# Kernel tuning notes

Measured on AMD Instinct MI355X. Metric: run time of the kernel, lower is better.

## Reference

```python
import jax, jax.numpy as jnp
import numpy as np
import math

B, N, E, D = 8, 2048, 2048, 128
MAX_K = 8
HYPER_DIM = 128
LN_EPS = 1e-5


def _sinusoidal_pe(max_pos, dim):
    pe = np.zeros((max_pos, dim), dtype=np.float32)
    position = np.arange(max_pos, dtype=np.float32)[:, None]
    div_term = np.exp(np.arange(0, dim, 2, dtype=np.float32) * (-math.log(10000.0) / dim))
    pe[:, 0::2] = np.sin(position * div_term)
    pe[:, 1::2] = np.cos(position * div_term)
    return jnp.asarray(pe)


def setup_inputs() -> dict:
    key = jax.random.key(0)
    ks = jax.random.split(key, 24)
    s = 0.05
    inp = {
        'x_v': jax.random.normal(ks[0], (B, N, D), jnp.float32),
        'x_e': jax.random.normal(ks[1], (B, E, D), jnp.float32),
        'incidence': (jax.random.uniform(ks[2], (B, N, E), jnp.float32) < 0.01).astype(jnp.float32),
        'suffix_normalizer': jax.random.uniform(ks[3], (B, N), jnp.float32) * 20.0,
        'edge_orders': 1 + jax.random.randint(ks[4], (B, E), 0, MAX_K),
        'node_mask': jax.random.randint(ks[5], (B, N), 0, 2) > 0,
        'edge_mask': jax.random.randint(ks[6], (B, E), 0, 2) > 0,
        'pe1_table': _sinusoidal_pe(MAX_K + 1, D),
        'pe2_table': _sinusoidal_pe(2, D),
        'bias_b': jax.random.uniform(ks[7], (1, D), jnp.float32, -1, 1) / math.sqrt(D),
    }
    i = 8
    for m in ('mlp1', 'mlp2', 'mlp3'):
        inp[m + '_W1'] = jax.random.normal(ks[i], (D, HYPER_DIM), jnp.float32) * s; i += 1
        inp[m + '_b1'] = jnp.zeros((HYPER_DIM,), jnp.float32)
        inp[m + '_W2'] = jax.random.normal(ks[i], (HYPER_DIM, D), jnp.float32) * s; i += 1
        inp[m + '_b2'] = jnp.zeros((D,), jnp.float32)
    for n in ('norm1', 'norm2', 'norm3'):
        inp[n + '_g'] = jnp.ones((D,), jnp.float32)
        inp[n + '_b'] = jnp.zeros((D,), jnp.float32)
    return inp


def _ln(x, g, b):
    mu = jnp.mean(x, axis=-1, keepdims=True)
    var = jnp.mean(jnp.square(x - mu), axis=-1, keepdims=True)
    return (x - mu) * jax.lax.rsqrt(var + LN_EPS) * g + b


def _mlp(x, W1, b1, W2, b2):
    return jax.nn.relu(x @ W1 + b1) @ W2 + b2


def reference(x_v, x_e, incidence, suffix_normalizer, edge_orders, node_mask, edge_mask,
              pe1_table, pe2_table, bias_b,
              mlp1_W1, mlp1_b1, mlp1_W2, mlp1_b2,
              mlp2_W1, mlp2_b1, mlp2_W2, mlp2_b2,
              mlp3_W1, mlp3_b1, mlp3_W2, mlp3_b2,
              norm1_g, norm1_b, norm2_g, norm2_b, norm3_g, norm3_b):
    nm = node_mask[..., None]  # [B,N,1]
    em = edge_mask[..., None]  # [B,E,1]
    x_v = jnp.where(nm, x_v, 0.0)
    x_e = jnp.where(em, x_e, 0.0)
    pe1_k1 = pe1_table[1][None, None, :]          # [1,1,D]
    pe1_k = pe1_table[edge_orders]                # [B,E,D]
    x_v = x_v + _mlp(_ln(x_v, norm1_g, norm1_b) + pe1_k1, mlp1_W1, mlp1_b1, mlp1_W2, mlp1_b2)
    x_e = x_e + _mlp(_ln(x_e, norm1_g, norm1_b) + pe1_k, mlp1_W1, mlp1_b1, mlp1_W2, mlp1_b2)
    x_v = jnp.where(nm, x_v, 0.0)
    x_e = jnp.where(em, x_e, 0.0)
    agg = jnp.einsum('bne,bed->bnd', incidence, x_e)
    x1 = x_v + agg / (1.0 + suffix_normalizer[..., None])
    pe2_s1 = pe2_table[1][None, None, :]
    x1 = x1 + _mlp(_ln(x1, norm2_g, norm2_b) + pe2_s1, mlp2_W1, mlp2_b1, mlp2_W2, mlp2_b2)
    x = jnp.where(nm, x1, 0.0)
    x = x + _mlp(_ln(x, norm3_g, norm3_b), mlp3_W1, mlp3_b1, mlp3_W2, mlp3_b2)
    x = x + bias_b
    x = jnp.where(nm, x, 0.0)
    return x
```

## Files before the change

kernel.cpp:

```cpp
#include <hip/hip_runtime.h>
#include <stdint.h>

#define BB 8
#define NN 2048
#define EE 2048
#define DD 128
#define ROWS 32
#define RBP 132
#define NTHREADS 256
#define WMAT_U32 8192

typedef __attribute__((ext_vector_type(8))) short bf16x8;
typedef __attribute__((ext_vector_type(4))) float f32x4;

__device__ inline unsigned bf16rne(float f) {
    unsigned u = __float_as_uint(f);
    return (u + 0x7fffu + ((u >> 16) & 1u)) >> 16;
}
__device__ inline float bf16lo(unsigned u) { return __uint_as_float(u << 16); }
__device__ inline float bf16hi(unsigned u) { return __uint_as_float(u & 0xffff0000u); }

#define SWZ(b) ((b) ^ ((((b) >> 8) & 7) << 4))

struct __align__(16) Smem {
    float rowbuf[ROWS][RBP];
    unsigned h[ROWS * DD / 2];
    unsigned scw[4][64];
    int rmask[ROWS];
    int ords[ROWS];
};

__global__ __launch_bounds__(NTHREADS) void convert_w_kernel(
    const float* __restrict__ W11, const float* __restrict__ W12,
    const float* __restrict__ W21, const float* __restrict__ W22,
    const float* __restrict__ W31, const float* __restrict__ W32,
    unsigned* __restrict__ WT) {
    int tid = blockIdx.x * NTHREADS + threadIdx.x;
    if (tid >= 6 * WMAT_U32) return;
    int mat = tid >> 13;
    int idx = tid & (WMAT_U32 - 1);
    int n = idx >> 6, j = idx & 63;
    const float* W = mat == 0 ? W11 : mat == 1 ? W12 : mat == 2 ? W21
                   : mat == 3 ? W22 : mat == 4 ? W31 : W32;
    float a = W[(2 * j) * DD + n];
    float b = W[(2 * j + 1) * DD + n];
    WT[tid] = bf16rne(a) | (bf16rne(b) << 16);
}

__device__ inline void block_load_rows(Smem& s, const float* __restrict__ src,
                                       const int* __restrict__ mask) {
    int t = threadIdx.x;
    for (int idx = t; idx < ROWS * 32; idx += NTHREADS) {
        int r = idx >> 5, c4 = (idx & 31) * 4;
        float4 v = make_float4(0.f, 0.f, 0.f, 0.f);
        if (mask[r] != 0) v = *(const float4*)&src[r * DD + c4];
        *(float4*)&s.rowbuf[r][c4] = v;
    }
    __syncthreads();
}

__device__ inline void block_ln(Smem& s, const float* __restrict__ gw,
                                const float* __restrict__ bw,
                                const float* __restrict__ pe_base, bool per_row_pe) {
    int t = threadIdx.x;
    int gr = t >> 3, g = t & 7;
    int base = g * 16;
    float x[16];
    float4* xp = (float4*)x;
    xp[0] = *(const float4*)&s.rowbuf[gr][base + 0];
    xp[1] = *(const float4*)&s.rowbuf[gr][base + 4];
    xp[2] = *(const float4*)&s.rowbuf[gr][base + 8];
    xp[3] = *(const float4*)&s.rowbuf[gr][base + 12];
    float s1 = 0.f, s2 = 0.f;
    #pragma unroll
    for (int i = 0; i < 16; i++) { s1 += x[i]; s2 += x[i] * x[i]; }
    #pragma unroll
    for (int off = 1; off < 8; off <<= 1) {
        s1 += __shfl_xor(s1, off, 64);
        s2 += __shfl_xor(s2, off, 64);
    }
    float mu = s1 * (1.f / 128.f);
    float var = s2 * (1.f / 128.f) - mu * mu;
    float rstd = rsqrtf(var + 1e-5f);
    const float* pe = nullptr;
    if (pe_base) pe = per_row_pe ? (pe_base + (size_t)s.ords[gr] * DD) : pe_base;
    unsigned p[8];
    #pragma unroll
    for (int j = 0; j < 8; j++) {
        int k0 = base + 2 * j;
        float v0 = (x[2 * j] - mu) * rstd * gw[k0] + bw[k0];
        float v1 = (x[2 * j + 1] - mu) * rstd * gw[k0 + 1] + bw[k0 + 1];
        if (pe) { v0 += pe[k0]; v1 += pe[k0 + 1]; }
        p[j] = bf16rne(v0) | (bf16rne(v1) << 16);
    }
    char* hb = (char*)s.h;
    int byte0 = gr * 256 + g * 32;
    uint4 lo = make_uint4(p[0], p[1], p[2], p[3]);
    uint4 hi = make_uint4(p[4], p[5], p[6], p[7]);
    *(uint4*)(hb + SWZ(byte0)) = lo;
    *(uint4*)(hb + SWZ(byte0 + 16)) = hi;
    __syncthreads();
}

template <bool TO_H>
__device__ inline void block_mm(Smem& s, const unsigned* __restrict__ WT,
                                const float* __restrict__ bias) {
    int t = threadIdx.x;
    int w = t >> 6, l = t & 63;
    int lm = l & 15, lk = l >> 4;
    bf16x8 bfr[2][4];
    const uint4* wt4 = (const uint4*)WT;
    #pragma unroll
    for (int nbl = 0; nbl < 2; nbl++) {
        int n = w * 32 + nbl * 16 + lm;
        #pragma unroll
        for (int kb = 0; kb < 4; kb++) {
            uint4 u = wt4[n * 16 + kb * 4 + lk];
            bfr[nbl][kb] = *(bf16x8*)&u;
        }
    }
    const char* hb = (const char*)s.h;
    bf16x8 afr[2][4];
    #pragma unroll
    for (int mb = 0; mb < 2; mb++) {
        int row = mb * 16 + lm;
        #pragma unroll
        for (int kb = 0; kb < 4; kb++) {
            afr[mb][kb] = *(const bf16x8*)(hb + SWZ(row * 256 + kb * 64 + lk * 16));
        }
    }
    f32x4 acc[2][2];
    #pragma unroll
    for (int mb = 0; mb < 2; mb++)
        #pragma unroll
        for (int nbl = 0; nbl < 2; nbl++)
            acc[mb][nbl] = (f32x4){0.f, 0.f, 0.f, 0.f};
    #pragma unroll
    for (int kb = 0; kb < 4; kb++)
        #pragma unroll
        for (int mb = 0; mb < 2; mb++)
            #pragma unroll
            for (int nbl = 0; nbl < 2; nbl++)
                acc[mb][nbl] = __builtin_amdgcn_mfma_f32_16x16x32_bf16(
                    afr[mb][kb], bfr[nbl][kb], acc[mb][nbl], 0, 0, 0);
    float bcol0 = bias[w * 32 + lm];
    float bcol1 = bias[w * 32 + 16 + lm];
    __syncthreads();
    if (TO_H) {
        char* hw = (char*)s.h;
        #pragma unroll
        for (int mb = 0; mb < 2; mb++)
            #pragma unroll
            for (int nbl = 0; nbl < 2; nbl++) {
                int col = w * 32 + nbl * 16 + lm;
                float bc = nbl ? bcol1 : bcol0;
                #pragma unroll
                for (int j = 0; j < 4; j++) {
                    int row = mb * 16 + lk * 4 + j;
                    float v = fmaxf(acc[mb][nbl][j] + bc, 0.f);
                    *(unsigned short*)(hw + SWZ(row * 256 + col * 2)) =
                        (unsigned short)bf16rne(v);
                }
            }
    } else {
        #pragma unroll
        for (int mb = 0; mb < 2; mb++)
            #pragma unroll
            for (int nbl = 0; nbl < 2; nbl++) {
                int col = w * 32 + nbl * 16 + lm;
                float bc = nbl ? bcol1 : bcol0;
                #pragma unroll
                for (int j = 0; j < 4; j++) {
                    int row = mb * 16 + lk * 4 + j;
                    s.rowbuf[row][col] += acc[mb][nbl][j] + bc;
                }
            }
    }
    __syncthreads();
}

__device__ inline void block_gather(Smem& s, int rowbase, int bb,
                                    const float* __restrict__ inc,
                                    const unsigned* __restrict__ e2pk,
                                    const float* __restrict__ sn) {
    int t = threadIdx.x;
    int w = t >> 6, l = t & 63;
    unsigned long long lmlt = (1ull << l) - 1ull;
    unsigned* sc = s.scw[w];
    const unsigned* e2b = e2pk + (size_t)bb * (EE * (DD / 2));
    for (int r = w; r < ROWS; r += 4) {
        if (s.rmask[r] == 0) continue;
        int grow = rowbase + r;
        const float4* ir = (const float4*)(inc + (size_t)grow * EE);
        float4 v[8];
        #pragma unroll
        for (int i = 0; i < 8; i++) v[i] = ir[l + 64 * i];
        int total = 0;
        #pragma unroll
        for (int i = 0; i < 8; i++) {
            #pragma unroll
            for (int c = 0; c < 4; c++) {
                float val = (c == 0) ? v[i].x : (c == 1) ? v[i].y : (c == 2) ? v[i].z : v[i].w;
                bool nz = (val != 0.f);
                unsigned long long msk = __ballot(nz);
                if (nz) {
                    int pos = total + __popcll(msk & lmlt);
                    if (pos < 64) sc[pos] = (unsigned)((l + 64 * i) * 4 + c);
                }
                total += __popcll(msk);
            }
        }
        if (total > 64) total = 64;
        asm volatile("s_waitcnt lgkmcnt(0)" ::: "memory");
        unsigned pk = (l < total) ? sc[l] : 0u;
        float ax = 0.f, ay = 0.f;
        for (int j0 = 0; j0 < total; j0 += 8) {
            int nn = total - j0;
            unsigned uv[8];
            #pragma unroll
            for (int u = 0; u < 8; u++) {
                unsigned e = __shfl(pk, j0 + u, 64);
                uv[u] = (u < nn) ? e2b[(size_t)e * 64 + l] : 0u;
            }
            #pragma unroll
            for (int u = 0; u < 8; u++) { ax += bf16lo(uv[u]); ay += bf16hi(uv[u]); }
        }
        float inv = 1.f / (1.f + sn[grow]);
        float2* rb = (float2*)&s.rowbuf[r][2 * l];
        float2 cur = *rb;
        cur.x += ax * inv;
        cur.y += ay * inv;
        *rb = cur;
    }
    __syncthreads();
}

__global__ __launch_bounds__(NTHREADS) void edge_kernel(
    const float* __restrict__ x_e, const int* __restrict__ emask,
    const int* __restrict__ eord, const float* __restrict__ pe1,
    const float* __restrict__ n1g, const float* __restrict__ n1b,
    const unsigned* __restrict__ WT,
    const float* __restrict__ b11, const float* __restrict__ b12,
    unsigned* __restrict__ e2pk) {
    __shared__ Smem s;
    int bid = blockIdx.x;
    int bb = bid & 7;
    int e0 = (bid >> 3) * ROWS;
    int rowbase = bb * EE + e0;
    int t = threadIdx.x;
    if (t < ROWS) {
        s.rmask[t] = emask[rowbase + t];
        int o = eord[rowbase + t];
        s.ords[t] = o < 0 ? 0 : (o > 8 ? 8 : o);
    }
    block_load_rows(s, x_e + (size_t)rowbase * DD, emask + rowbase);
    block_ln(s, n1g, n1b, pe1, true);
    block_mm<true>(s, WT + 0 * WMAT_U32, b11);
    block_mm<false>(s, WT + 1 * WMAT_U32, b12);
    unsigned* dst = e2pk + (size_t)rowbase * (DD / 2);
    for (int idx = t; idx < ROWS * 16; idx += NTHREADS) {
        int r = idx >> 4, q = idx & 15;
        uint4 o = make_uint4(0u, 0u, 0u, 0u);
        if (s.rmask[r] != 0) {
            const float* rp = &s.rowbuf[r][q * 8];
            o.x = bf16rne(rp[0]) | (bf16rne(rp[1]) << 16);
            o.y = bf16rne(rp[2]) | (bf16rne(rp[3]) << 16);
            o.z = bf16rne(rp[4]) | (bf16rne(rp[5]) << 16);
            o.w = bf16rne(rp[6]) | (bf16rne(rp[7]) << 16);
        }
        *(uint4*)&dst[r * 64 + q * 4] = o;
    }
}

__global__ __launch_bounds__(NTHREADS) void node_kernel(
    const float* __restrict__ x_v, const int* __restrict__ nmask,
    const float* __restrict__ inc, const float* __restrict__ sn,
    const float* __restrict__ pe1, const float* __restrict__ pe2,
    const float* __restrict__ biasb,
    const float* __restrict__ n1g, const float* __restrict__ n1b,
    const float* __restrict__ n2g, const float* __restrict__ n2b,
    const float* __restrict__ n3g, const float* __restrict__ n3b,
    const unsigned* __restrict__ WT,
    const float* __restrict__ b11, const float* __restrict__ b12,
    const float* __restrict__ b21, const float* __restrict__ b22,
    const float* __restrict__ b31, const float* __restrict__ b32,
    const unsigned* __restrict__ e2pk, float* __restrict__ out) {
    __shared__ Smem s;
    int bid = blockIdx.x;
    int bb = bid & 7;
    int n0 = (bid >> 3) * ROWS;
    int rowbase = bb * NN + n0;
    int t = threadIdx.x;
    if (t < ROWS) s.rmask[t] = nmask[rowbase + t];
    block_load_rows(s, x_v + (size_t)rowbase * DD, nmask + rowbase);
    block_ln(s, n1g, n1b, pe1 + DD, false);
    block_mm<true>(s, WT + 0 * WMAT_U32, b11);
    block_mm<false>(s, WT + 1 * WMAT_U32, b12);
    block_gather(s, rowbase, bb, inc, e2pk, sn);
    block_ln(s, n2g, n2b, pe2 + DD, false);
    block_mm<true>(s, WT + 2 * WMAT_U32, b21);
    block_mm<false>(s, WT + 3 * WMAT_U32, b22);
    block_ln(s, n3g, n3b, nullptr, false);
    block_mm<true>(s, WT + 4 * WMAT_U32, b31);
    block_mm<false>(s, WT + 5 * WMAT_U32, b32);
    for (int idx = t; idx < ROWS * 32; idx += NTHREADS) {
        int r = idx >> 5, c4 = (idx & 31) * 4;
        float4 v = make_float4(0.f, 0.f, 0.f, 0.f);
        if (s.rmask[r] != 0) {
            v = *(const float4*)&s.rowbuf[r][c4];
            float4 bbv = *(const float4*)&biasb[c4];
            v.x += bbv.x; v.y += bbv.y; v.z += bbv.z; v.w += bbv.w;
        }
        *(float4*)&out[(size_t)(rowbase + r) * DD + c4] = v;
    }
}

extern "C" void kernel_launch(void* const* d_in, const int* in_sizes, int n_in,
                              void* d_out, int out_size, void* d_ws, size_t ws_size,
                              hipStream_t stream) {
    const float* x_v   = (const float*)d_in[0];
    const float* x_e   = (const float*)d_in[1];
    const float* inc   = (const float*)d_in[2];
    const float* sn    = (const float*)d_in[3];
    const int*   eord  = (const int*)d_in[4];
    const int*   nmask = (const int*)d_in[5];
    const int*   emask = (const int*)d_in[6];
    const float* pe1   = (const float*)d_in[7];
    const float* pe2   = (const float*)d_in[8];
    const float* biasb = (const float*)d_in[9];
    const float* W11   = (const float*)d_in[10];
    const float* b11   = (const float*)d_in[11];
    const float* W12   = (const float*)d_in[12];
    const float* b12   = (const float*)d_in[13];
    const float* W21   = (const float*)d_in[14];
    const float* b21   = (const float*)d_in[15];
    const float* W22   = (const float*)d_in[16];
    const float* b22   = (const float*)d_in[17];
    const float* W31   = (const float*)d_in[18];
    const float* b31   = (const float*)d_in[19];
    const float* W32   = (const float*)d_in[20];
    const float* b32   = (const float*)d_in[21];
    const float* n1g   = (const float*)d_in[22];
    const float* n1b   = (const float*)d_in[23];
    const float* n2g   = (const float*)d_in[24];
    const float* n2b   = (const float*)d_in[25];
    const float* n3g   = (const float*)d_in[26];
    const float* n3b   = (const float*)d_in[27];

    unsigned* e2pk = (unsigned*)d_ws;
    unsigned* WT   = e2pk + (size_t)BB * EE * (DD / 2);
    float*    out  = (float*)d_out;

    dim3 blk(NTHREADS);
    convert_w_kernel<<<dim3((6 * WMAT_U32 + NTHREADS - 1) / NTHREADS), blk, 0, stream>>>(
        W11, W12, W21, W22, W31, W32, WT);
    edge_kernel<<<dim3(BB * EE / ROWS), blk, 0, stream>>>(
        x_e, emask, eord, pe1, n1g, n1b, WT, b11, b12, e2pk);
    node_kernel<<<dim3(BB * NN / ROWS), blk, 0, stream>>>(
        x_v, nmask, inc, sn, pe1, pe2, biasb,
        n1g, n1b, n2g, n2b, n3g, n3b,
        WT, b11, b12, b21, b22, b31, b32,
        e2pk, out);
}
```

Measured before the change: 68.61 us.

## Move incidence scan into edge kernel as extra blocks producing compact neighbor lists

The dense incidence scan that builds per-node nonzero edge lists moves out of the node kernel. It now runs in extra blocks appended to the edge kernel launch, so the 128 MiB incidence read can overlap with the edge MLP work. Lists and counts go to workspace, and the node kernel only reads the compact lists before gathering. This costs extra global writes and reads for the lists, and the edge-kernel blocks now compete with the scan blocks for bandwidth.

```diff
diff --git a/kernel.cpp b/kernel.cpp
--- a/kernel.cpp
+++ b/kernel.cpp
@@ -9,6 +9,8 @@
 #define RBP 132
 #define NTHREADS 256
 #define WMAT_U32 8192
+#define SCANB 2048
+#define LCAP 64
 
 typedef __attribute__((ext_vector_type(8))) short bf16x8;
 typedef __attribute__((ext_vector_type(4))) float f32x4;
@@ -179,18 +181,16 @@
     __syncthreads();
 }
 
-__device__ inline void block_gather(Smem& s, int rowbase, int bb,
-                                    const float* __restrict__ inc,
-                                    const unsigned* __restrict__ e2pk,
-                                    const float* __restrict__ sn) {
-    int t = threadIdx.x;
-    int w = t >> 6, l = t & 63;
+__device__ inline void scan_rows(Smem& s, const float* __restrict__ inc,
+                                 const int* __restrict__ nmask,
+                                 unsigned* __restrict__ lists, int* __restrict__ cnts,
+                                 int wid, int nwaves) {
+    int l = threadIdx.x & 63;
+    int w = threadIdx.x >> 6;
+    unsigned* sc = s.scw[w];
     unsigned long long lmlt = (1ull << l) - 1ull;
-    unsigned* sc = s.scw[w];
-    const unsigned* e2b = e2pk + (size_t)bb * (EE * (DD / 2));
-    for (int r = w; r < ROWS; r += 4) {
-        if (s.rmask[r] == 0) continue;
-        int grow = rowbase + r;
+    for (int grow = wid; grow < BB * NN; grow += nwaves) {
+        if (nmask[grow] == 0) continue;
         const float4* ir = (const float4*)(inc + (size_t)grow * EE);
         float4 v[8];
         #pragma unroll
@@ -205,17 +205,37 @@
                 unsigned long long msk = __ballot(nz);
                 if (nz) {
                     int pos = total + __popcll(msk & lmlt);
-                    if (pos < 64) sc[pos] = (unsigned)((l + 64 * i) * 4 + c);
+                    if (pos < LCAP) sc[pos] = (unsigned)((l + 64 * i) * 4 + c);
                 }
                 total += __popcll(msk);
             }
         }
-        if (total > 64) total = 64;
+        if (total > LCAP) total = LCAP;
         asm volatile("s_waitcnt lgkmcnt(0)" ::: "memory");
-        unsigned pk = (l < total) ? sc[l] : 0u;
+        if (l < 16) {
+            uint4 q = *(const uint4*)&sc[4 * l];
+            *(uint4*)&lists[(size_t)grow * LCAP + 4 * l] = q;
+        }
+        if (l == 0) cnts[grow] = total;
+    }
+}
+
+__device__ inline void block_gather(Smem& s, int rowbase, int bb,
+                                    const unsigned* __restrict__ lists,
+                                    const int* __restrict__ cnts,
+                                    const unsigned* __restrict__ e2pk,
+                                    const float* __restrict__ sn) {
+    int t = threadIdx.x;
+    int w = t >> 6, l = t & 63;
+    const unsigned* e2b = e2pk + (size_t)bb * (EE * (DD / 2));
+    for (int r = w; r < ROWS; r += 4) {
+        if (s.rmask[r] == 0) continue;
+        int grow = rowbase + r;
+        int cnt = cnts[grow];
+        unsigned pk = (l < cnt) ? lists[(size_t)grow * LCAP + l] : 0u;
         float ax = 0.f, ay = 0.f;
-        for (int j0 = 0; j0 < total; j0 += 8) {
-            int nn = total - j0;
+        for (int j0 = 0; j0 < cnt; j0 += 8) {
+            int nn = cnt - j0;
             unsigned uv[8];
             #pragma unroll
             for (int u = 0; u < 8; u++) {
@@ -235,19 +255,26 @@
     __syncthreads();
 }
 
-__global__ __launch_bounds__(NTHREADS) void edge_kernel(
+__global__ __launch_bounds__(NTHREADS) void edge_scan_kernel(
     const float* __restrict__ x_e, const int* __restrict__ emask,
     const int* __restrict__ eord, const float* __restrict__ pe1,
     const float* __restrict__ n1g, const float* __restrict__ n1b,
     const unsigned* __restrict__ WT,
     const float* __restrict__ b11, const float* __restrict__ b12,
-    unsigned* __restrict__ e2pk) {
+    const float* __restrict__ inc, const int* __restrict__ nmask,
+    unsigned* __restrict__ e2pk, unsigned* __restrict__ lists, int* __restrict__ cnts) {
     __shared__ Smem s;
     int bid = blockIdx.x;
+    const int EB = BB * EE / ROWS;
+    int t = threadIdx.x;
+    if (bid >= EB) {
+        int wid = (bid - EB) * 4 + (t >> 6);
+        scan_rows(s, inc, nmask, lists, cnts, wid, SCANB * 4);
+        return;
+    }
     int bb = bid & 7;
     int e0 = (bid >> 3) * ROWS;
     int rowbase = bb * EE + e0;
-    int t = threadIdx.x;
     if (t < ROWS) {
         s.rmask[t] = emask[rowbase + t];
         int o = eord[rowbase + t];
@@ -274,7 +301,7 @@
 
 __global__ __launch_bounds__(NTHREADS) void node_kernel(
     const float* __restrict__ x_v, const int* __restrict__ nmask,
-    const float* __restrict__ inc, const float* __restrict__ sn,
+    const float* __restrict__ sn,
     const float* __restrict__ pe1, const float* __restrict__ pe2,
     const float* __restrict__ biasb,
     const float* __restrict__ n1g, const float* __restrict__ n1b,
@@ -284,7 +311,8 @@
     const float* __restrict__ b11, const float* __restrict__ b12,
     const float* __restrict__ b21, const float* __restrict__ b22,
     const float* __restrict__ b31, const float* __restrict__ b32,
-    const unsigned* __restrict__ e2pk, float* __restrict__ out) {
+    const unsigned* __restrict__ e2pk, const unsigned* __restrict__ lists,
+    const int* __restrict__ cnts, float* __restrict__ out) {
     __shared__ Smem s;
     int bid = blockIdx.x;
     int bb = bid & 7;
@@ -296,7 +324,7 @@
     block_ln(s, n1g, n1b, pe1 + DD, false);
     block_mm<true>(s, WT + 0 * WMAT_U32, b11);
     block_mm<false>(s, WT + 1 * WMAT_U32, b12);
-    block_gather(s, rowbase, bb, inc, e2pk, sn);
+    block_gather(s, rowbase, bb, lists, cnts, e2pk, sn);
     block_ln(s, n2g, n2b, pe2 + DD, false);
     block_mm<true>(s, WT + 2 * WMAT_U32, b21);
     block_mm<false>(s, WT + 3 * WMAT_U32, b22);
@@ -347,18 +375,20 @@
     const float* n3g   = (const float*)d_in[26];
     const float* n3b   = (const float*)d_in[27];
 
-    unsigned* e2pk = (unsigned*)d_ws;
-    unsigned* WT   = e2pk + (size_t)BB * EE * (DD / 2);
-    float*    out  = (float*)d_out;
+    unsigned* e2pk  = (unsigned*)d_ws;
+    unsigned* WT    = e2pk + (size_t)BB * EE * (DD / 2);
+    unsigned* lists = WT + 6 * WMAT_U32;
+    int*      cnts  = (int*)(lists + (size_t)BB * NN * LCAP);
+    float*    out   = (float*)d_out;
 
     dim3 blk(NTHREADS);
     convert_w_kernel<<<dim3((6 * WMAT_U32 + NTHREADS - 1) / NTHREADS), blk, 0, stream>>>(
         W11, W12, W21, W22, W31, W32, WT);
-    edge_kernel<<<dim3(BB * EE / ROWS), blk, 0, stream>>>(
-        x_e, emask, eord, pe1, n1g, n1b, WT, b11, b12, e2pk);
+    edge_scan_kernel<<<dim3(BB * EE / ROWS + SCANB), blk, 0, stream>>>(
+        x_e, emask, eord, pe1, n1g, n1b, WT, b11, b12, inc, nmask, e2pk, lists, cnts);
     node_kernel<<<dim3(BB * NN / ROWS), blk, 0, stream>>>(
-        x_v, nmask, inc, sn, pe1, pe2, biasb,
+        x_v, nmask, sn, pe1, pe2, biasb,
         n1g, n1b, n2g, n2b, n3g, n3b,
         WT, b11, b12, b21, b22, b31, b32,
-        e2pk, out);
-}
+        e2pk, lists, cnts, out);
+}
```

Measured after the change: 64.43 us. 6.1% less time.
